# Kernel optimization log

Hardware: AMD Instinct MI355X
Metric: run time of the kernel (lower is better)

## Reference

```python
import jax, jax.numpy as jnp
import numpy as np

B, N = 128, 512            # graphs per batch, nodes (seq len) per graph
NODE_VOCAB, APP_VOCAB = 30000, 5000
D, R, K = 128, 512, 3      # embed_size, rec_embed dim, Chebyshev order
EPS = 1e-12


def setup_inputs() -> dict:
    key = jax.random.key(0)
    ks = jax.random.split(key, 8)
    return {
        # all tokens nonzero -> every position is a valid node (item > 0 filter passes)
        "input_seq": jax.random.randint(ks[0], (B, N), 1, NODE_VOCAB),
        "recd_token": jax.random.randint(ks[1], (B, N), 1, APP_VOCAB),
        "embed_table": jax.random.normal(ks[2], (NODE_VOCAB, D), jnp.float32) * 0.02,
        "rec_embed_table": jax.random.normal(ks[3], (APP_VOCAB, R), jnp.float32) * 0.02,
        "cheb_w1": jax.random.normal(ks[4], (K, D, D), jnp.float32) / np.sqrt(D),
        "cheb_b1": jnp.zeros((D,), jnp.float32),
        "cheb_w2": jax.random.normal(ks[5], (K, D, D), jnp.float32) / np.sqrt(D),
        "cheb_b2": jnp.zeros((D,), jnp.float32),
    }


def _prop_matrix(app_emb):
    """Per-sample scaled Laplacian L_hat = -D^{-1/2} A D^{-1/2}.

    app_emb: [B,N,R] (detached upstream, matching recd.detach() in the source).
    Adjacency: cosine-sim matrix, entries below the mean of the nonzero strict
    upper triangle zeroed. ChebConv receives edge_index only -> binary weights,
    self-loops removed, default lambda_max=2 -> L_hat = -A_norm.
    """
    app_feat = app_emb / jnp.maximum(
        jnp.linalg.norm(app_emb, axis=-1, keepdims=True), EPS)      # F.normalize dim=1
    A = jnp.einsum('bnr,bmr->bnm', app_feat, app_feat)              # [B,N,N]
    upper = jnp.triu(A, 1)
    cnt = jnp.sum(upper != 0, axis=(1, 2)).astype(A.dtype)
    mean = jnp.sum(upper, axis=(1, 2)) / jnp.maximum(cnt, 1.0)      # [B]
    A = jnp.where(A < mean[:, None, None], 0.0, A)
    adj = (A != 0).astype(A.dtype) * (1.0 - jnp.eye(N, dtype=A.dtype))  # binary, no self-loops
    deg = adj.sum(-1)                                               # [B,N]
    dinv = jnp.where(deg > 0, jax.lax.rsqrt(jnp.maximum(deg, EPS)), 0.0)
    return -(dinv[:, :, None] * adj * dinv[:, None, :])             # [B,N,N]


def _cheb(x, S, w, b):
    # Chebyshev recurrence T0=x, T1=Sx, T2=2S T1 - T0
    tx0 = x
    tx1 = jnp.einsum('bnm,bmd->bnd', S, tx0)
    tx2 = 2.0 * jnp.einsum('bnm,bmd->bnd', S, tx1) - tx0
    return (jnp.einsum('bnd,de->bne', tx0, w[0])
            + jnp.einsum('bnd,de->bne', tx1, w[1])
            + jnp.einsum('bnd,de->bne', tx2, w[2]) + b)


def reference(input_seq, recd_token, embed_table, rec_embed_table,
              cheb_w1, cheb_b1, cheb_w2, cheb_b2):
    app_emb = rec_embed_table[recd_token]                           # [B,N,R]
    # adjacency built from detached embeddings (recd.detach() in source)
    S = jax.lax.stop_gradient(_prop_matrix(jax.lax.stop_gradient(app_emb)))
    x = embed_table[input_seq]                                      # [B,N,D]
    x = jax.nn.relu(_cheb(x, S, cheb_w1, cheb_b1))
    x = jax.nn.relu(_cheb(x, S, cheb_w2, cheb_b2))
    out = jnp.concatenate([x, app_emb], axis=-1)                    # [B,N,D+R]
    return out.reshape(B * N, D + R)                                # Batch'ed node features
```

## Files before the change

kernel.cpp:

```cpp
#include <hip/hip_runtime.h>
#include <hip/hip_bf16.h>

typedef __attribute__((ext_vector_type(8))) unsigned short ushort8;
typedef __attribute__((ext_vector_type(4))) unsigned short bf16x4;
typedef __attribute__((ext_vector_type(8))) short short8;
typedef __attribute__((ext_vector_type(4))) float f32x4;
typedef __attribute__((ext_vector_type(2))) unsigned long long u64x2;

#define DEV __device__ __forceinline__

DEV unsigned short f2bf(float f) {
    unsigned u = __builtin_bit_cast(unsigned, f);
    return (unsigned short)((u + 0x7fffu + ((u >> 16) & 1u)) >> 16);
}
DEV float bf2f(unsigned short h) {
    unsigned u = ((unsigned)h) << 16;
    return __builtin_bit_cast(float, u);
}
DEV float wred(float v) {
#pragma unroll
    for (int m = 32; m > 0; m >>= 1) v += __shfl_xor(v, m, 64);
    return v;
}

constexpr int N_ = 512, D_ = 128, R_ = 512;
constexpr long NN2 = (long)N_ * N_;

DEV void gll16(const void* g, void* l) {
    __builtin_amdgcn_global_load_lds(
        (const __attribute__((address_space(1))) unsigned*)g,
        (__attribute__((address_space(3))) unsigned*)l, 16, 0, 0);
}


__global__ __launch_bounds__(256) void k_front(const int* __restrict__ recd,
                                               const float* __restrict__ rtab,
                                               const int* __restrict__ seq,
                                               const float* __restrict__ etab,
                                               const float* __restrict__ w1,
                                               const float* __restrict__ w2,
                                               float* __restrict__ out,
                                               unsigned short* __restrict__ x,
                                               unsigned short* __restrict__ wT,
                                               unsigned short* __restrict__ rtb,
                                               float* __restrict__ rnorm) {
    int bid = blockIdx.x, tid = threadIdx.x;
    if (bid < 16384) {
        int lane = tid & 63, w = tid >> 6;
        long r = (long)bid * 4 + w;
        int tok = recd[r];
        const float* src = rtab + (long)tok * R_;
        int j = lane * 8;
        float4 v0 = *(const float4*)(src + j);
        float4 v1 = *(const float4*)(src + j + 4);
        float ssq = v0.x*v0.x + v0.y*v0.y + v0.z*v0.z + v0.w*v0.w
                  + v1.x*v1.x + v1.y*v1.y + v1.z*v1.z + v1.w*v1.w;
        ssq = wred(ssq);
        float* o = out + r * 640 + 128 + j;
        *(float4*)o = v0;
        *(float4*)(o + 4) = v1;
        if (lane == 0) rnorm[r] = 1.0f / fmaxf(sqrtf(ssq), 1e-12f);
    } else if (bid < 20480) {
        long e8 = ((long)(bid - 16384) * 256 + tid) * 8;
        long r = e8 >> 7;
        int d0 = (int)(e8 & 127);
        int tok = seq[r];
        const float* src = etab + (long)tok * D_ + d0;
        float4 v0 = *(const float4*)src, v1 = *(const float4*)(src + 4);
        ushort8 u;
        u[0]=f2bf(v0.x); u[1]=f2bf(v0.y); u[2]=f2bf(v0.z); u[3]=f2bf(v0.w);
        u[4]=f2bf(v1.x); u[5]=f2bf(v1.y); u[6]=f2bf(v1.z); u[7]=f2bf(v1.w);
        *(ushort8*)(x + e8) = u;
    } else if (bid < 20864) {
        int o = (bid - 20480) * 256 + tid;
        int l = o / 49152;
        int rr = o - l * 49152;
        int mat = rr >> 14;
        int e2 = rr & 16383;
        int e = e2 >> 7, d = e2 & 127;
        const float* w = l ? w2 : w1;
        float v;
        if (mat == 0)      v = w[d * 128 + e] - w[32768 + d * 128 + e];
        else if (mat == 1) v = w[16384 + d * 128 + e];
        else               v = 2.0f * w[32768 + d * 128 + e];
        wT[o] = f2bf(v);
    } else {
        long e8 = ((long)(bid - 20864) * 256 + tid) * 8;
        float4 v0 = *(const float4*)(rtab + e8), v1 = *(const float4*)(rtab + e8 + 4);
        ushort8 u;
        u[0]=f2bf(v0.x); u[1]=f2bf(v0.y); u[2]=f2bf(v0.z); u[3]=f2bf(v0.w);
        u[4]=f2bf(v1.x); u[5]=f2bf(v1.y); u[6]=f2bf(v1.z); u[7]=f2bf(v1.w);
        *(ushort8*)(rtb + e8) = u;
    }
}


DEV void stage_rowmajor(const unsigned short* base, long ld, int k0,
                        unsigned short* dst, int tid) {
#pragma unroll
    for (int i = 0; i < 4; ++i) {
        int u = i * 256 + tid;
        int r = u >> 3, c = (u & 7) * 8;
        gll16(base + (long)r * ld + k0 + c,
              dst + i * 2048 + (tid & 448) * 8);
    }
}

DEV void stage_panel128(const unsigned short* base, int k0,
                        unsigned short* dst, int tid) {
#pragma unroll
    for (int i = 0; i < 8; ++i) {
        int u = i * 256 + tid;
        int r = u >> 4, c = (u & 15) * 8;
        gll16(base + (long)r * 512 + k0 + c,
              dst + i * 2048 + (tid & 448) * 8);
    }
}

DEV void stage_gather(const unsigned short* tab, const int* toks, int k0,
                      unsigned short* dst, int tid) {
#pragma unroll
    for (int i = 0; i < 4; ++i) {
        int u = i * 256 + tid;
        int r = u >> 3, c = (u & 7) * 8;
        gll16(tab + (long)toks[r] * 512 + k0 + c,
              dst + i * 2048 + (tid & 448) * 8);
    }
}

DEV void gemm_bt_core(const unsigned short* Abase, long ldA,
                      const unsigned short* Bbase, long ldB, int K,
                      unsigned short* As, unsigned short* Bs,
                      f32x4 acc[4][4], bool dual) {
    int tid = threadIdx.x, lane = tid & 63, wave = tid >> 6;
    int wm = wave >> 1, wn = wave & 1;
    int fr = lane & 15, ko = (lane >> 4) * 8;
    const unsigned short* Bsrc = dual ? Bs : As;
    for (int k0 = 0; k0 < K; k0 += 64) {
        __syncthreads();
        stage_rowmajor(Abase, ldA, k0, As, tid);
        if (dual) stage_rowmajor(Bbase, ldB, k0, Bs, tid);
        __syncthreads();
#pragma unroll
        for (int ks = 0; ks < 2; ++ks) {
            short8 a[4], b[4];
#pragma unroll
            for (int m = 0; m < 4; ++m)
                a[m] = *(const short8*)(As + (wm * 64 + m * 16 + fr) * 64 + ks * 32 + ko);
#pragma unroll
            for (int n = 0; n < 4; ++n)
                b[n] = *(const short8*)(Bsrc + (wn * 64 + n * 16 + fr) * 64 + ks * 32 + ko);
#pragma unroll
            for (int m = 0; m < 4; ++m)
#pragma unroll
                for (int n = 0; n < 4; ++n)
                    acc[m][n] = __builtin_amdgcn_mfma_f32_16x16x32_bf16(
                        a[m], b[n], acc[m][n], 0, 0, 0);
        }
    }
}


__global__ __launch_bounds__(256) void k_adj(const unsigned short* __restrict__ rtb,
                                             const int* __restrict__ recd,
                                             const float* __restrict__ rnorm,
                                             unsigned short* __restrict__ Abf,
                                             float* __restrict__ psum,
                                             float* __restrict__ pcnt) {
    __shared__ __align__(16) unsigned short As[128 * 64], Bs[128 * 64];
    __shared__ int toks[256];
    __shared__ float sred[4], cred[4];
    int g = blockIdx.x;
    int r8 = g & 7, q = g >> 3;
    int q10 = q / 10;
    int b = r8 + (q10 << 3);
    int t = q - q10 * 10;
    int tm = (t < 4) ? 0 : (t < 7) ? 1 : (t < 9) ? 2 : 3;
    int tn = t - (tm * (9 - tm)) / 2 + tm;
    bool diag = (tm == tn);
    int tid = threadIdx.x, lane = tid & 63, wave = tid >> 6;
    if (tid < 128) toks[tid] = recd[b * 512 + tm * 128 + tid];
    else           toks[tid] = recd[b * 512 + tn * 128 + (tid - 128)];
    int wm = wave >> 1, wn = wave & 1;
    int fr = lane & 15, ko = (lane >> 4) * 8;
    f32x4 acc[4][4] = {};
    for (int k0 = 0; k0 < 512; k0 += 64) {
        __syncthreads();
        stage_gather(rtb, toks, k0, As, tid);
        if (!diag) stage_gather(rtb, toks + 128, k0, Bs, tid);
        __syncthreads();
        const unsigned short* Bsrc = diag ? As : Bs;
#pragma unroll
        for (int ks = 0; ks < 2; ++ks) {
            short8 a[4], bb[4];
#pragma unroll
            for (int m = 0; m < 4; ++m)
                a[m] = *(const short8*)(As + (wm * 64 + m * 16 + fr) * 64 + ks * 32 + ko);
#pragma unroll
            for (int n = 0; n < 4; ++n)
                bb[n] = *(const short8*)(Bsrc + (wn * 64 + n * 16 + fr) * 64 + ks * 32 + ko);
#pragma unroll
            for (int m = 0; m < 4; ++m)
#pragma unroll
                for (int n = 0; n < 4; ++n)
                    acc[m][n] = __builtin_amdgcn_mfma_f32_16x16x32_bf16(
                        a[m], bb[n], acc[m][n], 0, 0, 0);
        }
    }
    float s = 0.f, c = 0.f;
    unsigned short* Ab = Abf + (long)b * NN2;
    const float* rnb = rnorm + (long)b * 512;
#pragma unroll
    for (int m = 0; m < 4; ++m) {
        int gi0 = tm * 128 + wm * 64 + m * 16 + (lane >> 4) * 4;
        float4 rni = *(const float4*)(rnb + gi0);
#pragma unroll
        for (int n = 0; n < 4; ++n) {
            int gj = tn * 128 + wn * 64 + n * 16 + fr;
            float rj = rnb[gj];
            f32x4 v = acc[m][n];
            bf16x4 tw;
#pragma unroll
            for (int qq = 0; qq < 4; ++qq) {
                int gi = gi0 + qq;
                float vv = v[qq] * (&rni.x)[qq] * rj;
                unsigned short bv = f2bf(vv);
                Ab[(long)gi * N_ + gj] = bv;
                tw[qq] = bv;
                if (gj > gi) {
                    s += vv;
                    c += (vv != 0.0f) ? 1.0f : 0.0f;
                }
            }
            if (!diag)
                *(bf16x4*)(Ab + (long)gj * N_ + gi0) = tw;
        }
    }
    s = wred(s);
    c = wred(c);
    if (lane == 0) { sred[wave] = s; cred[wave] = c; }
    __syncthreads();
    if (tid == 0) {
        psum[b * 16 + t] = sred[0] + sred[1] + sred[2] + sred[3];
        pcnt[b * 16 + t] = cred[0] + cred[1] + cred[2] + cred[3];
    }
}

__global__ __launch_bounds__(256) void k_degtrs(unsigned short* __restrict__ Abf,
                                                const float* __restrict__ psum,
                                                const float* __restrict__ pcnt,
                                                const unsigned short* __restrict__ xin,
                                                float* __restrict__ dinv,
                                                unsigned short* __restrict__ pT) {
    __shared__ unsigned char mb[4][64];
    __shared__ float sdinv[64];
    __shared__ unsigned short t[64 * 128];
    int bid = blockIdx.x;
    int b = bid >> 3, tn = bid & 7;
    int tid = threadIdx.x, lane = tid & 63, w = tid >> 6;
    float s = 0.f, c = 0.f;
#pragma unroll
    for (int k = 0; k < 10; ++k) { s += psum[b * 16 + k]; c += pcnt[b * 16 + k]; }
    float m = s / fmaxf(c, 1.0f);
#pragma unroll 1
    for (int i = 0; i < 16; ++i) {
        int rl = w * 16 + i;
        long r = (long)b * 512 + tn * 64 + rl;
        int ig = tn * 64 + rl;
        ushort8 v = *(const ushort8*)(Abf + r * 512 + lane * 8);
        unsigned byt = 0;
        int cnt = 0;
#pragma unroll
        for (int k = 0; k < 8; ++k) {
            float f = bf2f(v[k]);
            int j = lane * 8 + k;
            bool keep = (f >= m) && (f != 0.0f) && (j != ig);
            byt |= (keep ? 1u : 0u) << k;
            cnt += keep ? 1 : 0;
        }
        mb[w][lane] = (unsigned char)byt;
        float fc = wred((float)cnt);
        if (lane < 8) {
            unsigned long long mword = *(const unsigned long long*)&mb[w][lane * 8];
            *(unsigned long long*)((unsigned char*)Abf + r * 1024 + lane * 8) = mword;
        }
        if (lane == 8) {
            float dv = (fc > 0.f) ? rsqrtf(fc) : 0.f;
            dinv[r] = dv;
            sdinv[rl] = dv;
        }
    }
    __syncthreads();
    const unsigned short* ib = xin + ((long)b * 512 + tn * 64) * 128;
    unsigned short* ob = pT + (long)b * 65536 + tn * 64;
#pragma unroll
    for (int i = 0; i < 4; ++i) {
        int u = i * 256 + tid;
        int n = u >> 4, g = u & 15;
        float sc = sdinv[n];
        ushort8 v = *(const ushort8*)(ib + n * 128 + g * 8);
        ushort8 sv;
#pragma unroll
        for (int tt = 0; tt < 8; ++tt) sv[tt] = f2bf(bf2f(v[tt]) * sc);
        int gs = g ^ ((n >> 3) & 7);
        *(ushort8*)(t + n * 128 + gs * 8) = sv;
    }
    __syncthreads();
#pragma unroll
    for (int i = 0; i < 4; ++i) {
        int u = i * 256 + tid;
        int d = u >> 3, n8 = (u & 7) * 8;
        ushort8 v;
#pragma unroll
        for (int tt = 0; tt < 8; ++tt) {
            int n = n8 + tt;
            int g = (d >> 3) ^ ((n >> 3) & 7);
            v[tt] = t[n * 128 + g * 8 + (d & 7)];
        }
        *(ushort8*)(ob + (long)d * 512 + n8) = v;
    }
}

__global__ __launch_bounds__(256) void k_sxm(const unsigned short* __restrict__ Abf,
                                             const float* __restrict__ dinv,
                                             const unsigned short* __restrict__ pT,
                                             unsigned short* __restrict__ outN,
                                             unsigned short* __restrict__ outT) {
    __shared__ __align__(16) unsigned short Bs[128 * 128];
    __shared__ __align__(8) unsigned short lut4[16 * 4];
    int tid = threadIdx.x, lane = tid & 63, wave = tid >> 6;
    if (tid < 16) {
        unsigned long long e = 0;
#pragma unroll
        for (int j = 0; j < 4; ++j)
            if ((tid >> j) & 1) e |= 0x3F80ull << (16 * j);
        *(unsigned long long*)(lut4 + tid * 4) = e;
    }
    int g = blockIdx.x;
    int r = g & 7, q = g >> 3;
    int b = r + ((q >> 2) << 3);
    int tm = q & 3;
    int wm = wave >> 1, wn = wave & 1;
    int fr = lane & 15, ko = (lane >> 4) * 8;
    const unsigned char* mbase = (const unsigned char*)Abf + (long)b * 524288;
    const unsigned short* pb = pT + (long)b * 65536;
    f32x4 acc[4][4] = {};
    for (int k0 = 0; k0 < 512; k0 += 128) {
        __syncthreads();
        stage_panel128(pb, k0, Bs, tid);
        u64x2 mw[4];
#pragma unroll
        for (int m = 0; m < 4; ++m) {
            int row = tm * 128 + wm * 64 + m * 16 + fr;
            mw[m] = *(const u64x2*)(mbase + (long)row * 1024 + (k0 >> 3));
        }
        __syncthreads();
#pragma unroll
        for (int ks = 0; ks < 4; ++ks) {
            short8 a4[4], b4[4];
#pragma unroll
            for (int m = 0; m < 4; ++m) {
                unsigned w32 = (unsigned)(mw[m][ks >> 1] >> ((ks & 1) * 32));
                unsigned byt = (w32 >> ko) & 255u;
                unsigned long long lo = *(const unsigned long long*)(lut4 + (byt & 15u) * 4);
                unsigned long long hi = *(const unsigned long long*)(lut4 + (byt >> 4) * 4);
                u64x2 tt; tt[0] = lo; tt[1] = hi;
                a4[m] = __builtin_bit_cast(short8, tt);
            }
#pragma unroll
            for (int n = 0; n < 4; ++n)
                b4[n] = *(const short8*)(Bs + (wn * 64 + n * 16 + fr) * 128 + ks * 32 + ko);
#pragma unroll
            for (int m = 0; m < 4; ++m)
#pragma unroll
                for (int n = 0; n < 4; ++n)
                    acc[m][n] = __builtin_amdgcn_mfma_f32_16x16x32_bf16(
                        a4[m], b4[n], acc[m][n], 0, 0, 0);
        }
    }
    unsigned short* on = outN + (long)b * 65536;
#pragma unroll
    for (int m = 0; m < 4; ++m) {
        int gi0 = tm * 128 + wm * 64 + m * 16 + ((lane >> 4) << 2);
        float4 dv = *(const float4*)(dinv + (long)b * 512 + gi0);
#pragma unroll
        for (int n = 0; n < 4; ++n) {
            int gj = wn * 64 + n * 16 + fr;
            bf16x4 tw;
#pragma unroll
            for (int qq = 0; qq < 4; ++qq) {
                float dq = (&dv.x)[qq];
                float t1v = -dq * acc[m][n][qq];
                on[(long)(gi0 + qq) * 128 + gj] = f2bf(t1v);
                tw[qq] = f2bf(dq * t1v);
            }
            *(bf16x4*)(outT + (long)b * 65536 + (long)gj * 512 + gi0) = tw;
        }
    }
}

template <int LAYER>
__global__ __launch_bounds__(256) void k_sxp(const unsigned short* __restrict__ Abf,
                                             const float* __restrict__ dinv,
                                             const unsigned short* __restrict__ pTin,
                                             const unsigned short* __restrict__ t0,
                                             const unsigned short* __restrict__ t1,
                                             const unsigned short* __restrict__ wTl,
                                             const float* __restrict__ bias,
                                             unsigned short* __restrict__ ybf,
                                             unsigned short* __restrict__ pTout,
                                             float* __restrict__ out) {
    __shared__ __align__(16) unsigned short AsBs[128 * 128];
    __shared__ __align__(16) unsigned short uLds[128 * 132];
    __shared__ __align__(8) unsigned short lut4[16 * 4];
    int tid = threadIdx.x, lane = tid & 63, wave = tid >> 6;
    if (tid < 16) {
        unsigned long long e = 0;
#pragma unroll
        for (int j = 0; j < 4; ++j)
            if ((tid >> j) & 1) e |= 0x3F80ull << (16 * j);
        *(unsigned long long*)(lut4 + tid * 4) = e;
    }
    int g = blockIdx.x;
    int r = g & 7, q = g >> 3;
    int b = r + ((q >> 2) << 3);
    int tm = q & 3;
    int wm = wave >> 1, wn = wave & 1;
    int fr = lane & 15, ko = (lane >> 4) * 8;
    {
        const unsigned char* mbase = (const unsigned char*)Abf + (long)b * 524288;
        const unsigned short* pb = pTin + (long)b * 65536;
        f32x4 acc[4][4] = {};
        for (int k0 = 0; k0 < 512; k0 += 128) {
            __syncthreads();
            stage_panel128(pb, k0, AsBs, tid);
            u64x2 mw[4];
#pragma unroll
            for (int m = 0; m < 4; ++m) {
                int row = tm * 128 + wm * 64 + m * 16 + fr;
                mw[m] = *(const u64x2*)(mbase + (long)row * 1024 + (k0 >> 3));
            }
            __syncthreads();
#pragma unroll
            for (int ks = 0; ks < 4; ++ks) {
                short8 a4[4], b4[4];
#pragma unroll
                for (int m = 0; m < 4; ++m) {
                    unsigned w32 = (unsigned)(mw[m][ks >> 1] >> ((ks & 1) * 32));
                    unsigned byt = (w32 >> ko) & 255u;
                    unsigned long long lo = *(const unsigned long long*)(lut4 + (byt & 15u) * 4);
                    unsigned long long hi = *(const unsigned long long*)(lut4 + (byt >> 4) * 4);
                    u64x2 tt; tt[0] = lo; tt[1] = hi;
                    a4[m] = __builtin_bit_cast(short8, tt);
                }
#pragma unroll
                for (int n = 0; n < 4; ++n)
                    b4[n] = *(const short8*)(AsBs + (wn * 64 + n * 16 + fr) * 128 + ks * 32 + ko);
#pragma unroll
                for (int m = 0; m < 4; ++m)
#pragma unroll
                    for (int n = 0; n < 4; ++n)
                        acc[m][n] = __builtin_amdgcn_mfma_f32_16x16x32_bf16(
                            a4[m], b4[n], acc[m][n], 0, 0, 0);
            }
        }
#pragma unroll
        for (int m = 0; m < 4; ++m) {
            int li0 = wm * 64 + m * 16 + ((lane >> 4) << 2);
            float4 dv = *(const float4*)(dinv + (long)b * 512 + tm * 128 + li0);
#pragma unroll
            for (int n = 0; n < 4; ++n) {
                int gj = wn * 64 + n * 16 + fr;
#pragma unroll
                for (int qq = 0; qq < 4; ++qq)
                    uLds[(li0 + qq) * 132 + gj] = f2bf(-(&dv.x)[qq] * acc[m][n][qq]);
            }
        }
    }
    unsigned short* As = AsBs;
    unsigned short* Bs = AsBs + 8192;
    long row0 = (long)b * 512 + tm * 128;
    f32x4 acc2[4][4] = {};
    gemm_bt_core(t0 + row0 * D_, D_, wTl,          D_, D_, As, Bs, acc2, true);
    gemm_bt_core(t1 + row0 * D_, D_, wTl + 16384,  D_, D_, As, Bs, acc2, true);
    for (int s2 = 0; s2 < 2; ++s2) {
        __syncthreads();
        stage_rowmajor(wTl + 32768, 128, s2 * 64, Bs, tid);
        __syncthreads();
#pragma unroll
        for (int ks = 0; ks < 2; ++ks) {
            short8 a[4], bfr[4];
#pragma unroll
            for (int m = 0; m < 4; ++m)
                a[m] = *(const short8*)(uLds + (wm * 64 + m * 16 + fr) * 132 + s2 * 64 + ks * 32 + ko);
#pragma unroll
            for (int n = 0; n < 4; ++n)
                bfr[n] = *(const short8*)(Bs + (wn * 64 + n * 16 + fr) * 64 + ks * 32 + ko);
#pragma unroll
            for (int m = 0; m < 4; ++m)
#pragma unroll
                for (int n = 0; n < 4; ++n)
                    acc2[m][n] = __builtin_amdgcn_mfma_f32_16x16x32_bf16(
                        a[m], bfr[n], acc2[m][n], 0, 0, 0);
        }
    }
#pragma unroll
    for (int m = 0; m < 4; ++m) {
        long gr0 = row0 + wm * 64 + m * 16 + ((lane >> 4) << 2);
        float4 dv;
        if (LAYER == 1) dv = *(const float4*)(dinv + gr0);
#pragma unroll
        for (int n = 0; n < 4; ++n) {
            int gj = wn * 64 + n * 16 + (lane & 15);
            bf16x4 tw;
#pragma unroll
            for (int qq = 0; qq < 4; ++qq) {
                long gr = gr0 + qq;
                float v = fmaxf(acc2[m][n][qq] + bias[gj], 0.0f);
                if (LAYER == 1) {
                    ybf[gr * D_ + gj] = f2bf(v);
                    tw[qq] = f2bf((&dv.x)[qq] * v);
                } else {
                    out[gr * 640 + gj] = v;
                }
            }
            if (LAYER == 1)
                *(bf16x4*)(pTout + (gr0 >> 9) * 65536 + (long)gj * 512 + (gr0 & 511)) = tw;
        }
    }
}


extern "C" void kernel_launch(void* const* d_in, const int* in_sizes, int n_in,
                              void* d_out, int out_size, void* d_ws, size_t ws_size,
                              hipStream_t stream) {
    const int* seq    = (const int*)d_in[0];
    const int* recd   = (const int*)d_in[1];
    const float* etab = (const float*)d_in[2];
    const float* rtab = (const float*)d_in[3];
    const float* w1   = (const float*)d_in[4];
    const float* b1   = (const float*)d_in[5];
    const float* w2   = (const float*)d_in[6];
    const float* b2   = (const float*)d_in[7];
    float* out = (float*)d_out;
    char* ws = (char*)d_ws;

    if (ws_size < 151470592u) return;

    unsigned short* Abf  = (unsigned short*)(ws);
    unsigned short* pTa  = (unsigned short*)(ws + 67108864);
    unsigned short* pTb  = (unsigned short*)(ws + 83886080);
    unsigned short* t1   = (unsigned short*)(ws + 100663296);
    unsigned short* rtb  = (unsigned short*)(ws + 117440512);
    float* rnorm         = (float*)(ws + 122683392);
    unsigned short* xbf  = (unsigned short*)(ws + 134217728);
    unsigned short* wT   = (unsigned short*)(ws + 150994944);
    float* psum = (float*)(ws + 151191552);
    float* pcnt = (float*)(ws + 151199744);
    float* dinv = (float*)(ws + 151208448);

    k_front<<<22114, 256, 0, stream>>>(recd, rtab, seq, etab, w1, w2,
                                       out, xbf, wT, rtb, rnorm);
    k_adj<<<1280, 256, 0, stream>>>(rtb, recd, rnorm, Abf, psum, pcnt);
    k_degtrs<<<1024, 256, 0, stream>>>(Abf, psum, pcnt, xbf, dinv, pTa);
    k_sxm<<<512, 256, 0, stream>>>(Abf, dinv, pTa, t1, pTb);
    k_sxp<1><<<512, 256, 0, stream>>>(Abf, dinv, pTb, xbf, t1, wT, b1,
                                      xbf, pTa, nullptr);
    k_sxm<<<512, 256, 0, stream>>>(Abf, dinv, pTa, t1, pTb);
    k_sxp<2><<<512, 256, 0, stream>>>(Abf, dinv, pTb, xbf, t1, wT + 49152, b2,
                                      nullptr, nullptr, out);
}
```

Baseline: 225.9 us.

## Stage full per-graph panel once in LDS and use 512-thread blocks over half-graphs

The S·X kernels now use 512-thread blocks that each cover 256 rows (half a graph) and load the entire 128x512 transposed panel into padded LDS once. This replaces the per-k-step restaging and the barriers inside the K loop. The dense weight GEMM epilogue is rewritten with 256-row staging helpers, and the degree/transpose kernel remaps blocks so graphs spread across XCDs. This should cut redundant panel loads and synchronisation, but it uses about 130KB of LDS per block, so occupancy drops to one block per CU, and the grid is halved to 256 blocks.

```diff
diff --git a/kernel.cpp b/kernel.cpp
--- a/kernel.cpp
+++ b/kernel.cpp
@@ -25,6 +25,8 @@
 
 constexpr int N_ = 512, D_ = 128, R_ = 512;
 constexpr long NN2 = (long)N_ * N_;
+constexpr int PSTR = 520;
+constexpr int USTR = 136;
 
 DEV void gll16(const void* g, void* l) {
     __builtin_amdgcn_global_load_lds(
@@ -106,17 +108,6 @@
     }
 }
 
-DEV void stage_panel128(const unsigned short* base, int k0,
-                        unsigned short* dst, int tid) {
-#pragma unroll
-    for (int i = 0; i < 8; ++i) {
-        int u = i * 256 + tid;
-        int r = u >> 4, c = (u & 15) * 8;
-        gll16(base + (long)r * 512 + k0 + c,
-              dst + i * 2048 + (tid & 448) * 8);
-    }
-}
-
 DEV void stage_gather(const unsigned short* tab, const int* toks, int k0,
                       unsigned short* dst, int tid) {
 #pragma unroll
@@ -128,35 +119,24 @@
     }
 }
 
-DEV void gemm_bt_core(const unsigned short* Abase, long ldA,
-                      const unsigned short* Bbase, long ldB, int K,
-                      unsigned short* As, unsigned short* Bs,
-                      f32x4 acc[4][4], bool dual) {
-    int tid = threadIdx.x, lane = tid & 63, wave = tid >> 6;
-    int wm = wave >> 1, wn = wave & 1;
-    int fr = lane & 15, ko = (lane >> 4) * 8;
-    const unsigned short* Bsrc = dual ? Bs : As;
-    for (int k0 = 0; k0 < K; k0 += 64) {
-        __syncthreads();
-        stage_rowmajor(Abase, ldA, k0, As, tid);
-        if (dual) stage_rowmajor(Bbase, ldB, k0, Bs, tid);
-        __syncthreads();
-#pragma unroll
-        for (int ks = 0; ks < 2; ++ks) {
-            short8 a[4], b[4];
-#pragma unroll
-            for (int m = 0; m < 4; ++m)
-                a[m] = *(const short8*)(As + (wm * 64 + m * 16 + fr) * 64 + ks * 32 + ko);
-#pragma unroll
-            for (int n = 0; n < 4; ++n)
-                b[n] = *(const short8*)(Bsrc + (wn * 64 + n * 16 + fr) * 64 + ks * 32 + ko);
-#pragma unroll
-            for (int m = 0; m < 4; ++m)
-#pragma unroll
-                for (int n = 0; n < 4; ++n)
-                    acc[m][n] = __builtin_amdgcn_mfma_f32_16x16x32_bf16(
-                        a[m], b[n], acc[m][n], 0, 0, 0);
-        }
+
+DEV void stageA256(const unsigned short* base, int k0, unsigned short* dst, int tid) {
+    int w = tid >> 6;
+#pragma unroll
+    for (int i = 0; i < 4; ++i) {
+        int u = i * 512 + tid;
+        int r = u >> 3, c = (u & 7) * 8;
+        gll16(base + (long)r * 128 + k0 + c, dst + (i * 64 + w * 8) * 64);
+    }
+}
+
+DEV void stageB128(const unsigned short* base, int k0, unsigned short* dst, int tid) {
+    int w = tid >> 6;
+#pragma unroll
+    for (int i = 0; i < 2; ++i) {
+        int u = i * 512 + tid;
+        int r = u >> 3, c = (u & 7) * 8;
+        gll16(base + (long)r * 128 + k0 + c, dst + (i * 64 + w * 8) * 64);
     }
 }
 
@@ -256,7 +236,9 @@
     __shared__ float sdinv[64];
     __shared__ unsigned short t[64 * 128];
     int bid = blockIdx.x;
-    int b = bid >> 3, tn = bid & 7;
+    int q = bid >> 3, r8 = bid & 7;
+    int b = r8 + ((q >> 3) << 3);
+    int tn = q & 7;
     int tid = threadIdx.x, lane = tid & 63, w = tid >> 6;
     float s = 0.f, c = 0.f;
 #pragma unroll
@@ -321,14 +303,14 @@
     }
 }
 
-__global__ __launch_bounds__(256) void k_sxm(const unsigned short* __restrict__ Abf,
+__global__ __launch_bounds__(512) void k_sxm(const unsigned short* __restrict__ Abf,
                                              const float* __restrict__ dinv,
                                              const unsigned short* __restrict__ pT,
                                              unsigned short* __restrict__ outN,
                                              unsigned short* __restrict__ outT) {
-    __shared__ __align__(16) unsigned short Bs[128 * 128];
+    __shared__ __align__(16) unsigned short Ps[128 * PSTR];
     __shared__ __align__(8) unsigned short lut4[16 * 4];
-    int tid = threadIdx.x, lane = tid & 63, wave = tid >> 6;
+    int tid = threadIdx.x, lane = tid & 63, w = tid >> 6;
     if (tid < 16) {
         unsigned long long e = 0;
 #pragma unroll
@@ -337,30 +319,35 @@
         *(unsigned long long*)(lut4 + tid * 4) = e;
     }
     int g = blockIdx.x;
-    int r = g & 7, q = g >> 3;
-    int b = r + ((q >> 2) << 3);
-    int tm = q & 3;
-    int wm = wave >> 1, wn = wave & 1;
+    int xcd = g & 7, idx = g >> 3;
+    int b = xcd + ((idx >> 1) << 3);
+    int half = idx & 1;
+    int wm = w >> 1, wn = w & 1;
     int fr = lane & 15, ko = (lane >> 4) * 8;
     const unsigned char* mbase = (const unsigned char*)Abf + (long)b * 524288;
     const unsigned short* pb = pT + (long)b * 65536;
+#pragma unroll
+    for (int i = 0; i < 16; ++i) {
+        int r = i * 8 + w;
+        gll16(pb + (long)r * 512 + lane * 8, Ps + r * PSTR);
+    }
+    __syncthreads();
     f32x4 acc[4][4] = {};
+    int rowbase = half * 256 + wm * 64;
+#pragma unroll 1
     for (int k0 = 0; k0 < 512; k0 += 128) {
-        __syncthreads();
-        stage_panel128(pb, k0, Bs, tid);
         u64x2 mw[4];
 #pragma unroll
         for (int m = 0; m < 4; ++m) {
-            int row = tm * 128 + wm * 64 + m * 16 + fr;
+            int row = rowbase + m * 16 + fr;
             mw[m] = *(const u64x2*)(mbase + (long)row * 1024 + (k0 >> 3));
         }
-        __syncthreads();
-#pragma unroll
-        for (int ks = 0; ks < 4; ++ks) {
+#pragma unroll
+        for (int kss = 0; kss < 4; ++kss) {
             short8 a4[4], b4[4];
 #pragma unroll
             for (int m = 0; m < 4; ++m) {
-                unsigned w32 = (unsigned)(mw[m][ks >> 1] >> ((ks & 1) * 32));
+                unsigned w32 = (unsigned)(mw[m][kss >> 1] >> ((kss & 1) * 32));
                 unsigned byt = (w32 >> ko) & 255u;
                 unsigned long long lo = *(const unsigned long long*)(lut4 + (byt & 15u) * 4);
                 unsigned long long hi = *(const unsigned long long*)(lut4 + (byt >> 4) * 4);
@@ -369,7 +356,7 @@
             }
 #pragma unroll
             for (int n = 0; n < 4; ++n)
-                b4[n] = *(const short8*)(Bs + (wn * 64 + n * 16 + fr) * 128 + ks * 32 + ko);
+                b4[n] = *(const short8*)(Ps + (wn * 64 + n * 16 + fr) * PSTR + k0 + kss * 32 + ko);
 #pragma unroll
             for (int m = 0; m < 4; ++m)
 #pragma unroll
@@ -381,7 +368,7 @@
     unsigned short* on = outN + (long)b * 65536;
 #pragma unroll
     for (int m = 0; m < 4; ++m) {
-        int gi0 = tm * 128 + wm * 64 + m * 16 + ((lane >> 4) << 2);
+        int gi0 = half * 256 + wm * 64 + m * 16 + ((lane >> 4) << 2);
         float4 dv = *(const float4*)(dinv + (long)b * 512 + gi0);
 #pragma unroll
         for (int n = 0; n < 4; ++n) {
@@ -400,7 +387,7 @@
 }
 
 template <int LAYER>
-__global__ __launch_bounds__(256) void k_sxp(const unsigned short* __restrict__ Abf,
+__global__ __launch_bounds__(512) void k_sxp(const unsigned short* __restrict__ Abf,
                                              const float* __restrict__ dinv,
                                              const unsigned short* __restrict__ pTin,
                                              const unsigned short* __restrict__ t0,
@@ -410,10 +397,9 @@
                                              unsigned short* __restrict__ ybf,
                                              unsigned short* __restrict__ pTout,
                                              float* __restrict__ out) {
-    __shared__ __align__(16) unsigned short AsBs[128 * 128];
-    __shared__ __align__(16) unsigned short uLds[128 * 132];
+    __shared__ __align__(16) unsigned short lds[128 * PSTR];
     __shared__ __align__(8) unsigned short lut4[16 * 4];
-    int tid = threadIdx.x, lane = tid & 63, wave = tid >> 6;
+    int tid = threadIdx.x, lane = tid & 63, w = tid >> 6;
     if (tid < 16) {
         unsigned long long e = 0;
 #pragma unroll
@@ -422,31 +408,39 @@
         *(unsigned long long*)(lut4 + tid * 4) = e;
     }
     int g = blockIdx.x;
-    int r = g & 7, q = g >> 3;
-    int b = r + ((q >> 2) << 3);
-    int tm = q & 3;
-    int wm = wave >> 1, wn = wave & 1;
+    int xcd = g & 7, idx = g >> 3;
+    int b = xcd + ((idx >> 1) << 3);
+    int half = idx & 1;
+    int wm = w >> 1, wn = w & 1;
     int fr = lane & 15, ko = (lane >> 4) * 8;
+    unsigned short* As  = lds;
+    unsigned short* Bs  = lds + 16384;
+    unsigned short* uL  = lds + 24576;
     {
         const unsigned char* mbase = (const unsigned char*)Abf + (long)b * 524288;
         const unsigned short* pb = pTin + (long)b * 65536;
+#pragma unroll
+        for (int i = 0; i < 16; ++i) {
+            int r = i * 8 + w;
+            gll16(pb + (long)r * 512 + lane * 8, lds + r * PSTR);
+        }
+        __syncthreads();
         f32x4 acc[4][4] = {};
+        int rowbase = half * 256 + wm * 64;
+#pragma unroll 1
         for (int k0 = 0; k0 < 512; k0 += 128) {
-            __syncthreads();
-            stage_panel128(pb, k0, AsBs, tid);
             u64x2 mw[4];
 #pragma unroll
             for (int m = 0; m < 4; ++m) {
-                int row = tm * 128 + wm * 64 + m * 16 + fr;
+                int row = rowbase + m * 16 + fr;
                 mw[m] = *(const u64x2*)(mbase + (long)row * 1024 + (k0 >> 3));
             }
-            __syncthreads();
-#pragma unroll
-            for (int ks = 0; ks < 4; ++ks) {
+#pragma unroll
+            for (int kss = 0; kss < 4; ++kss) {
                 short8 a4[4], b4[4];
 #pragma unroll
                 for (int m = 0; m < 4; ++m) {
-                    unsigned w32 = (unsigned)(mw[m][ks >> 1] >> ((ks & 1) * 32));
+                    unsigned w32 = (unsigned)(mw[m][kss >> 1] >> ((kss & 1) * 32));
                     unsigned byt = (w32 >> ko) & 255u;
                     unsigned long long lo = *(const unsigned long long*)(lut4 + (byt & 15u) * 4);
                     unsigned long long hi = *(const unsigned long long*)(lut4 + (byt >> 4) * 4);
@@ -455,7 +449,7 @@
                 }
 #pragma unroll
                 for (int n = 0; n < 4; ++n)
-                    b4[n] = *(const short8*)(AsBs + (wn * 64 + n * 16 + fr) * 128 + ks * 32 + ko);
+                    b4[n] = *(const short8*)(lds + (wn * 64 + n * 16 + fr) * PSTR + k0 + kss * 32 + ko);
 #pragma unroll
                 for (int m = 0; m < 4; ++m)
 #pragma unroll
@@ -464,35 +458,61 @@
                             a4[m], b4[n], acc[m][n], 0, 0, 0);
             }
         }
+        __syncthreads();
 #pragma unroll
         for (int m = 0; m < 4; ++m) {
             int li0 = wm * 64 + m * 16 + ((lane >> 4) << 2);
-            float4 dv = *(const float4*)(dinv + (long)b * 512 + tm * 128 + li0);
+            float4 dv = *(const float4*)(dinv + (long)b * 512 + half * 256 + li0);
 #pragma unroll
             for (int n = 0; n < 4; ++n) {
                 int gj = wn * 64 + n * 16 + fr;
 #pragma unroll
                 for (int qq = 0; qq < 4; ++qq)
-                    uLds[(li0 + qq) * 132 + gj] = f2bf(-(&dv.x)[qq] * acc[m][n][qq]);
-            }
-        }
-    }
-    unsigned short* As = AsBs;
-    unsigned short* Bs = AsBs + 8192;
-    long row0 = (long)b * 512 + tm * 128;
+                    uL[(li0 + qq) * USTR + gj] = f2bf(-(&dv.x)[qq] * acc[m][n][qq]);
+            }
+        }
+    }
+    long row0 = (long)b * 512 + half * 256;
     f32x4 acc2[4][4] = {};
-    gemm_bt_core(t0 + row0 * D_, D_, wTl,          D_, D_, As, Bs, acc2, true);
-    gemm_bt_core(t1 + row0 * D_, D_, wTl + 16384,  D_, D_, As, Bs, acc2, true);
+#pragma unroll 1
+    for (int mat = 0; mat < 2; ++mat) {
+        const unsigned short* tsrc = (mat == 0) ? (t0 + row0 * D_) : (t1 + row0 * D_);
+        const unsigned short* wsrc = wTl + mat * 16384;
+#pragma unroll 1
+        for (int k0 = 0; k0 < 128; k0 += 64) {
+            __syncthreads();
+            stageA256(tsrc, k0, As, tid);
+            stageB128(wsrc, k0, Bs, tid);
+            __syncthreads();
+#pragma unroll
+            for (int ks = 0; ks < 2; ++ks) {
+                short8 a[4], bfr[4];
+#pragma unroll
+                for (int m = 0; m < 4; ++m)
+                    a[m] = *(const short8*)(As + (wm * 64 + m * 16 + fr) * 64 + ks * 32 + ko);
+#pragma unroll
+                for (int n = 0; n < 4; ++n)
+                    bfr[n] = *(const short8*)(Bs + (wn * 64 + n * 16 + fr) * 64 + ks * 32 + ko);
+#pragma unroll
+                for (int m = 0; m < 4; ++m)
+#pragma unroll
+                    for (int n = 0; n < 4; ++n)
+                        acc2[m][n] = __builtin_amdgcn_mfma_f32_16x16x32_bf16(
+                            a[m], bfr[n], acc2[m][n], 0, 0, 0);
+            }
+        }
+    }
+#pragma unroll 1
     for (int s2 = 0; s2 < 2; ++s2) {
         __syncthreads();
-        stage_rowmajor(wTl + 32768, 128, s2 * 64, Bs, tid);
+        stageB128(wTl + 32768, s2 * 64, Bs, tid);
         __syncthreads();
 #pragma unroll
         for (int ks = 0; ks < 2; ++ks) {
             short8 a[4], bfr[4];
 #pragma unroll
             for (int m = 0; m < 4; ++m)
-                a[m] = *(const short8*)(uLds + (wm * 64 + m * 16 + fr) * 132 + s2 * 64 + ks * 32 + ko);
+                a[m] = *(const short8*)(uL + (wm * 64 + m * 16 + fr) * USTR + s2 * 64 + ks * 32 + ko);
 #pragma unroll
             for (int n = 0; n < 4; ++n)
                 bfr[n] = *(const short8*)(Bs + (wn * 64 + n * 16 + fr) * 64 + ks * 32 + ko);
@@ -563,10 +583,10 @@
                                        out, xbf, wT, rtb, rnorm);
     k_adj<<<1280, 256, 0, stream>>>(rtb, recd, rnorm, Abf, psum, pcnt);
     k_degtrs<<<1024, 256, 0, stream>>>(Abf, psum, pcnt, xbf, dinv, pTa);
-    k_sxm<<<512, 256, 0, stream>>>(Abf, dinv, pTa, t1, pTb);
-    k_sxp<1><<<512, 256, 0, stream>>>(Abf, dinv, pTb, xbf, t1, wT, b1,
+    k_sxm<<<256, 512, 0, stream>>>(Abf, dinv, pTa, t1, pTb);
+    k_sxp<1><<<256, 512, 0, stream>>>(Abf, dinv, pTb, xbf, t1, wT, b1,
                                       xbf, pTa, nullptr);
-    k_sxm<<<512, 256, 0, stream>>>(Abf, dinv, pTa, t1, pTb);
-    k_sxp<2><<<512, 256, 0, stream>>>(Abf, dinv, pTb, xbf, t1, wT + 49152, b2,
+    k_sxm<<<256, 512, 0, stream>>>(Abf, dinv, pTa, t1, pTb);
+    k_sxp<2><<<256, 512, 0, stream>>>(Abf, dinv, pTb, xbf, t1, wT + 49152, b2,
                                       nullptr, nullptr, out);
 }
```

Measured after the change: 222.9 us. No clear change (-1.3%).
